# Kernel optimization log

Hardware: AMD Instinct MI355X
Metric: run time of the kernel (lower is better)

## Reference

```python
import jax, jax.numpy as jnp
import numpy as np

B, H, S, DK, DV = 4, 16, 2048, 64, 64
D_K = 64  # config.d_k used for scaling

def setup_inputs() -> dict:
    key = jax.random.key(0)
    kq, kk, kv, km = jax.random.split(key, 4)
    Q = jax.random.normal(kq, (B, H, S, DK), dtype=jnp.float32)
    K = jax.random.normal(kk, (B, H, S, DK), dtype=jnp.float32)
    V = jax.random.normal(kv, (B, H, S, DV), dtype=jnp.float32)
    attn_mask = jax.random.randint(km, (B, 1, S, S), 0, 2).astype(jnp.bool_)
    return {"Q": Q, "K": K, "V": V, "attn_mask": attn_mask}

def reference(Q, K, V, attn_mask):
    # scores: [B, H, S, S]
    scale = 1.0 / jnp.sqrt(jnp.asarray(D_K, dtype=Q.dtype))
    scores = jnp.einsum("bhqd,bhkd->bhqk", Q, K) * scale
    scores = jnp.where(attn_mask, jnp.asarray(-1e9, dtype=scores.dtype), scores)
    attn = jax.nn.softmax(scores, axis=-1)
    context = jnp.einsum("bhqk,bhkv->bhqv", attn, V)
    return context
```

## Files before the change

### kernel.cpp

```cpp
#include <hip/hip_runtime.h>
#include <hip/hip_bf16.h>
#include <math.h>

typedef __attribute__((ext_vector_type(4)))  float f32x4;
typedef __attribute__((ext_vector_type(16))) float f32x16;
typedef __attribute__((ext_vector_type(8)))  short short8_t;
typedef __attribute__((ext_vector_type(4)))  short short4_t;

constexpr int Bn = 4, Hn = 16, Sn = 2048, Dn = 64;
constexpr int MW  = Sn / 64;
constexpr int NKT = Sn / 64;

__device__ __forceinline__ unsigned short f2bf(float f) {
    union { float f; unsigned u; } x; x.f = f;
    unsigned r = x.u + 0x7fffu + ((x.u >> 16) & 1u);
    return (unsigned short)(r >> 16);
}
__device__ __forceinline__ int sw8(int row) { return (row ^ (row >> 3)) & 7; }
__device__ __forceinline__ float exp2fast(float x) {
#if __has_builtin(__builtin_amdgcn_exp2f)
    return __builtin_amdgcn_exp2f(x);
#else
    float r; asm("v_exp_f32 %0, %1" : "=v"(r) : "v"(x)); return r;
#endif
}
__device__ __forceinline__ float max3f(float a, float b, float c) {
    return fmaxf(fmaxf(a, b), c);
}
__device__ __forceinline__ f32x16 zero16() {
    f32x16 z;
#pragma unroll
    for (int i = 0; i < 16; ++i) z[i] = 0.f;
    return z;
}
__device__ __forceinline__ unsigned cvtpk(float lo, float hi_) {
    __hip_bfloat162 h2 = __float22bfloat162_rn(make_float2(lo, hi_));
    union { __hip_bfloat162 h; unsigned u; } u; u.h = h2;
    return u.u;
}
__device__ __forceinline__ void pswap(unsigned &x, unsigned &y) {
    asm("v_permlane32_swap_b32 %0, %1" : "+v"(x), "+v"(y));
}

__global__ __launch_bounds__(256) void pack_mask(const void* __restrict__ Mp,
                                                 unsigned long long* __restrict__ PM) {
    unsigned accv = 0;
    {
        const unsigned* mw = (const unsigned*)Mp;
#pragma unroll
        for (int i = 0; i < 8; ++i) accv |= (mw[i] & 0xFFFFFF00u);
    }
    const bool i32 = (accv == 0u);
    const int lane = threadIdx.x & 63;
    const int wv = (int)((blockIdx.x * 256 + threadIdx.x) >> 6);
    const int w0 = wv * (Bn * Sn * MW / 4096);
    const int* mi32 = (const int*)Mp;
    const unsigned char* mu8 = (const unsigned char*)Mp;
    for (int j = 0; j < 64; j += 4) {
        int m0, m1, m2, m3;
        if (i32) {
            m0 = mi32[(size_t)(w0 + j) * 64 + lane];
            m1 = mi32[(size_t)(w0 + j + 1) * 64 + lane];
            m2 = mi32[(size_t)(w0 + j + 2) * 64 + lane];
            m3 = mi32[(size_t)(w0 + j + 3) * 64 + lane];
        } else {
            m0 = mu8[(size_t)(w0 + j) * 64 + lane];
            m1 = mu8[(size_t)(w0 + j + 1) * 64 + lane];
            m2 = mu8[(size_t)(w0 + j + 2) * 64 + lane];
            m3 = mu8[(size_t)(w0 + j + 3) * 64 + lane];
        }
        unsigned long long b0 = __ballot(m0 != 0);
        unsigned long long b1 = __ballot(m1 != 0);
        unsigned long long b2 = __ballot(m2 != 0);
        unsigned long long b3 = __ballot(m3 != 0);
        if (lane == 0) {
            PM[w0 + j] = b0; PM[w0 + j + 1] = b1;
            PM[w0 + j + 2] = b2; PM[w0 + j + 3] = b3;
        }
    }
}

__global__ __launch_bounds__(256) void convKV(const float* __restrict__ K,
                                              const float* __restrict__ V,
                                              const void* __restrict__ Mp,
                                              unsigned short* __restrict__ Kb,
                                              unsigned short* __restrict__ Vt,
                                              unsigned long long* __restrict__ PM) {
    __shared__ unsigned short tile[64 * 72];
    const int bh = blockIdx.x, kt = blockIdx.y, t = threadIdx.x;

    {
        const float* ksrc = K + ((size_t)bh * Sn + kt * 64) * 64;
        unsigned short* kdst = Kb + ((size_t)bh * Sn + kt * 64) * 64;
#pragma unroll
        for (int j = 0; j < 2; ++j) {
            const int idx = j * 256 + t;
            f32x4 a = *(const f32x4*)(ksrc + idx * 8);
            f32x4 b = *(const f32x4*)(ksrc + idx * 8 + 4);
            short8_t h;
            h[0]=(short)f2bf(a[0]); h[1]=(short)f2bf(a[1]); h[2]=(short)f2bf(a[2]); h[3]=(short)f2bf(a[3]);
            h[4]=(short)f2bf(b[0]); h[5]=(short)f2bf(b[1]); h[6]=(short)f2bf(b[2]); h[7]=(short)f2bf(b[3]);
            *(short8_t*)(kdst + idx * 8) = h;
        }
    }

    {
        unsigned accv = 0;
        const unsigned* mw = (const unsigned*)Mp;
#pragma unroll
        for (int i = 0; i < 8; ++i) accv |= (mw[i] & 0xFFFFFF00u);
        const bool i32 = (accv == 0u);
        const int wv = t >> 6, lane = t & 63;
        const int base = (bh * NKT + kt) * 128 + wv * 32;
        const int* mi32 = (const int*)Mp;
        const unsigned char* mu8 = (const unsigned char*)Mp;
#pragma unroll 4
        for (int j = 0; j < 32; ++j) {
            int m = i32 ? mi32[(size_t)(base + j) * 64 + lane]
                        : (int)mu8[(size_t)(base + j) * 64 + lane];
            unsigned long long bal = __ballot(m != 0);
            if (lane == 0) PM[base + j] = bal;
        }
    }

    {
        const int k = t >> 2, vq = (t & 3) * 16;
        const float* src = V + ((size_t)bh * Sn + kt * 64 + k) * 64 + vq;
#pragma unroll
        for (int j = 0; j < 4; ++j) {
            f32x4 f = *(const f32x4*)(src + j * 4);
            short4_t h;
            h[0]=(short)f2bf(f[0]); h[1]=(short)f2bf(f[1]); h[2]=(short)f2bf(f[2]); h[3]=(short)f2bf(f[3]);
            *(short4_t*)&tile[k * 72 + vq + j * 4] = h;
        }
        __syncthreads();
#pragma unroll
        for (int j = 0; j < 2; ++j) {
            const int v = (t >> 3) + 32 * j;
            const int oct = t & 7;
            short8_t h;
#pragma unroll
            for (int i2 = 0; i2 < 8; ++i2) h[i2] = (short)tile[(oct * 8 + i2) * 72 + v];
            *(short8_t*)(Vt + ((size_t)bh * 64 + v) * Sn + kt * 64 + oct * 8) = h;
        }
    }
}

__global__ __launch_bounds__(256, 4) void sdpa_v3(
    const float* __restrict__ Qp, const unsigned short* __restrict__ Kb,
    const unsigned short* __restrict__ Vt, const unsigned long long* __restrict__ PM,
    float* __restrict__ Op)
{
    __shared__ __align__(16) char smem[32768];
    unsigned short* smK = (unsigned short*)smem;
    unsigned short* smV = (unsigned short*)(smem + 16384);
    unsigned short* smQ = (unsigned short*)smem;

    const int t = threadIdx.x;
    const int w = t >> 6;
    const int l = t & 63;
    const int ql = l & 31;
    const int hi = l >> 5;

    const int gid = blockIdx.x;
    const int lin = (gid & 7) * 128 + (gid >> 3);
    const int bh = lin >> 4;
    const int qb = lin & 15;
    const int b = bh >> 4;
    const int q0 = qb * 128;

    const unsigned short* KbB = Kb + (size_t)bh * Sn * 64;
    const unsigned short* VtB = Vt + (size_t)bh * 64 * Sn;

    {
        const float qscale = 0.125f * 1.44269504088896340736f;
        const float* Qbase = Qp + ((size_t)bh * Sn + q0) * Dn;
#pragma unroll
        for (int j = 0; j < 8; ++j) {
            const int flat = j * 256 + t;
            const int row = flat >> 4, c4 = (flat & 15) * 4;
            f32x4 f = *(const f32x4*)(Qbase + (size_t)flat * 4);
            short4_t h;
            h[0]=(short)f2bf(f[0]*qscale); h[1]=(short)f2bf(f[1]*qscale);
            h[2]=(short)f2bf(f[2]*qscale); h[3]=(short)f2bf(f[3]*qscale);
            *(short4_t*)&smQ[row * 72 + c4] = h;
        }
    }
    __syncthreads();
    short8_t qf[4];
    {
        const int rowl = w * 32 + ql;
#pragma unroll
        for (int tt = 0; tt < 4; ++tt)
            qf[tt] = *(const short8_t*)&smQ[rowl * 72 + tt * 16 + hi * 8];
    }
    __syncthreads();

    auto stage = [&](int kt, int buf) {
        const int row = t >> 3, oct = t & 7;
        const int row2 = row + 32;
        {
            const unsigned short* g = KbB + ((size_t)(kt * 64 + row)) * 64 + (oct ^ sw8(row)) * 8;
            __builtin_amdgcn_global_load_lds((const __attribute__((address_space(1))) unsigned int*)g,
                (__attribute__((address_space(3))) unsigned int*)(smK + buf * 4096 + t * 8), 16, 0, 0);
            const unsigned short* g2 = KbB + ((size_t)(kt * 64 + row2)) * 64 + (oct ^ sw8(row2)) * 8;
            __builtin_amdgcn_global_load_lds((const __attribute__((address_space(1))) unsigned int*)g2,
                (__attribute__((address_space(3))) unsigned int*)(smK + buf * 4096 + 2048 + t * 8), 16, 0, 0);
        }
        {
            const unsigned short* g = VtB + (size_t)row * Sn + kt * 64 + (oct ^ sw8(row)) * 8;
            __builtin_amdgcn_global_load_lds((const __attribute__((address_space(1))) unsigned int*)g,
                (__attribute__((address_space(3))) unsigned int*)(smV + buf * 4096 + t * 8), 16, 0, 0);
            const unsigned short* g2 = VtB + (size_t)row2 * Sn + kt * 64 + (oct ^ sw8(row2)) * 8;
            __builtin_amdgcn_global_load_lds((const __attribute__((address_space(1))) unsigned int*)g2,
                (__attribute__((address_space(3))) unsigned int*)(smV + buf * 4096 + 2048 + t * 8), 16, 0, 0);
        }
    };
    auto ldf = [&](const unsigned short* base, int row, int olog) -> short8_t {
        return *(const short8_t*)(base + row * 64 + (olog ^ sw8(row)) * 8);
    };

    f32x16 o0 = zero16(), o1 = zero16();
    float m_run = -INFINITY, l_run = 0.f;
    const int qrow = q0 + w * 32 + ql;
    const unsigned long long* pmrow = PM + ((size_t)b * Sn + qrow) * MW;

    stage(0, 0);
    __syncthreads();

    for (int kt = 0; kt < NKT; ++kt) {
        const int cur = kt & 1;
        if (kt + 1 < NKT) stage(kt + 1, cur ^ 1);
        const unsigned long long bits = pmrow[kt];
        const unsigned short* bK = smK + cur * 4096;
        const unsigned short* bV = smV + cur * 4096;

#pragma unroll
        for (int h = 0; h < 2; ++h) {
            f32x16 s = zero16();
            __builtin_amdgcn_s_setprio(1);
#pragma unroll
            for (int tt = 0; tt < 4; ++tt) {
                short8_t a0 = ldf(bK, 32 * h + ql, 2 * tt + hi);
                s = __builtin_amdgcn_mfma_f32_32x32x16_bf16(a0, qf[tt], s, 0, 0, 0);
            }
            __builtin_amdgcn_s_setprio(0);

            const unsigned w32 = (unsigned)(bits >> (32 * h)) >> (hi * 4);
#pragma unroll
            for (int r = 0; r < 16; ++r) {
                const int bp = 8 * (r >> 2) + (r & 3);
                s[r] = ((w32 >> bp) & 1u) ? -1e9f : s[r];
            }

            float mx = fmaxf(s[0], s[1]);
#pragma unroll
            for (int r = 2; r < 16; r += 2) mx = max3f(mx, s[r], s[r + 1]);
            mx = fmaxf(mx, __shfl_xor(mx, 32));

            if (!__all(mx - m_run <= 8.0f)) {
                const float mn = fmaxf(m_run, mx);
                const float corr = exp2fast(m_run - mn);
                m_run = mn;
                l_run *= corr;
#pragma unroll
                for (int r = 0; r < 16; ++r) {
                    const int qloc = (r & 3) + 8 * (r >> 2) + 4 * hi;
                    const float cr = __shfl(corr, qloc);
                    o0[r] *= cr; o1[r] *= cr;
                }
            }
#pragma unroll
            for (int r = 0; r < 16; ++r) s[r] = exp2fast(s[r] - m_run);

            {
                float p0 = 0.f, p1 = 0.f, p2 = 0.f, p3 = 0.f;
#pragma unroll
                for (int r = 0; r < 16; r += 4) {
                    p0 += s[r]; p1 += s[r + 1]; p2 += s[r + 2]; p3 += s[r + 3];
                }
                float rs = (p0 + p1) + (p2 + p3);
                rs += __shfl_xor(rs, 32);
                l_run += rs;
            }

            __builtin_amdgcn_s_setprio(1);
#pragma unroll
            for (int ksl = 0; ksl < 2; ++ksl) {
                const int off = ksl * 8;
                unsigned x0 = cvtpk(s[off],     s[off + 1]);
                unsigned x1 = cvtpk(s[off + 2], s[off + 3]);
                unsigned y0 = cvtpk(s[off + 4], s[off + 5]);
                unsigned y1 = cvtpk(s[off + 6], s[off + 7]);
                pswap(x0, y0);
                pswap(x1, y1);
                union { unsigned u[4]; short8_t v; } pa;
                pa.u[0] = x0; pa.u[1] = x1; pa.u[2] = y0; pa.u[3] = y1;
                const int ksg = 2 * h + ksl;
                short8_t vf0 = ldf(bV, ql,      2 * ksg + hi);
                short8_t vf1 = ldf(bV, 32 + ql, 2 * ksg + hi);
                o0 = __builtin_amdgcn_mfma_f32_32x32x16_bf16(pa.v, vf0, o0, 0, 0, 0);
                o1 = __builtin_amdgcn_mfma_f32_32x32x16_bf16(pa.v, vf1, o1, 0, 0, 0);
            }
            __builtin_amdgcn_s_setprio(0);
        }
        __syncthreads();
    }

    const float inv = 1.0f / l_run;
#pragma unroll
    for (int r = 0; r < 16; ++r) {
        const int qloc = (r & 3) + 8 * (r >> 2) + 4 * hi;
        const float iv = __shfl(inv, qloc);
        float* orow = Op + ((size_t)bh * Sn + q0 + w * 32 + qloc) * 64;
        orow[ql] = o0[r] * iv;
        orow[32 + ql] = o1[r] * iv;
    }
}

__global__ __launch_bounds__(512, 4) void sdpa_v2(
    const float* __restrict__ Qp, const float* __restrict__ Kp,
    const float* __restrict__ Vp, const void* __restrict__ Mp,
    const unsigned long long* __restrict__ PM, float* __restrict__ Op)
{
    __shared__ unsigned short lds_k[64 * 64];
    __shared__ unsigned short lds_vt[64 * 64];
    __shared__ unsigned short lds_p[8][16 * 64];

    const int t = threadIdx.x;
    const int wave = t >> 6;
    const int lane = t & 63;
    const int g = lane >> 4;
    const int c = lane & 15;

    const int gid = blockIdx.x;
    const int lin = (gid & 7) * 128 + (gid >> 3);
    const int bh = lin >> 4;
    const int qb = lin & 15;
    const int b = bh >> 4;
    const int q0 = qb * 128;

    bool m_i32 = true;
    if (!PM) {
        unsigned accv = 0;
        const unsigned* mw = (const unsigned*)Mp;
#pragma unroll
        for (int i = 0; i < 32; ++i) accv |= (mw[i] & 0xFFFFFF00u);
        m_i32 = (accv == 0u);
    }
    const int* mi32 = (const int*)Mp;
    const unsigned char* mu8 = (const unsigned char*)Mp;

    short8_t qf[2];
    {
        const float qscale = 0.125f * 1.44269504088896340736f;
        const float* qsrc = Qp + ((size_t)bh * Sn + q0 + wave * 16 + c) * Dn + g * 8;
#pragma unroll
        for (int h2 = 0; h2 < 2; ++h2) {
            f32x4 f0 = *(const f32x4*)(qsrc + h2 * 32);
            f32x4 f1 = *(const f32x4*)(qsrc + h2 * 32 + 4);
            short8_t v;
            v[0]=(short)f2bf(f0[0]*qscale); v[1]=(short)f2bf(f0[1]*qscale);
            v[2]=(short)f2bf(f0[2]*qscale); v[3]=(short)f2bf(f0[3]*qscale);
            v[4]=(short)f2bf(f1[0]*qscale); v[5]=(short)f2bf(f1[1]*qscale);
            v[6]=(short)f2bf(f1[2]*qscale); v[7]=(short)f2bf(f1[3]*qscale);
            qf[h2] = v;
        }
    }

    f32x4 o[4];
#pragma unroll
    for (int i = 0; i < 4; ++i) o[i] = (f32x4){0.f, 0.f, 0.f, 0.f};
    float m_run[4] = {-INFINITY, -INFINITY, -INFINITY, -INFINITY};
    float l_run[4] = {0.f, 0.f, 0.f, 0.f};

    const float* kbase = Kp + (size_t)bh * Sn * Dn;
    const float* vbase = Vp + (size_t)bh * Sn * Dn;
    const size_t mrow0 = (size_t)b * Sn + q0 + wave * 16 + g * 4;

    for (int kt = 0; kt < NKT; ++kt) {
        const int k0 = kt * 64;
        {
            const int key = t >> 3;
            const int d0 = (t & 7) * 8;
            const float* src = kbase + (size_t)(k0 + key) * Dn + d0;
            f32x4 f0 = *(const f32x4*)src;
            f32x4 f1 = *(const f32x4*)(src + 4);
            short8_t hv;
            hv[0]=(short)f2bf(f0[0]); hv[1]=(short)f2bf(f0[1]);
            hv[2]=(short)f2bf(f0[2]); hv[3]=(short)f2bf(f0[3]);
            hv[4]=(short)f2bf(f1[0]); hv[5]=(short)f2bf(f1[1]);
            hv[6]=(short)f2bf(f1[2]); hv[7]=(short)f2bf(f1[3]);
            *(short8_t*)&lds_k[key * 64 + (d0 ^ (sw8(key) << 3))] = hv;
        }
        {
            const int vv = t & 63;
            const int kq = (t >> 6) * 8;
            short8_t hv;
#pragma unroll
            for (int j = 0; j < 8; ++j)
                hv[j] = (short)f2bf(vbase[(size_t)(k0 + kq + j) * Dn + vv]);
            *(short8_t*)&lds_vt[vv * 64 + (kq ^ (sw8(vv) << 3))] = hv;
        }
        __syncthreads();

        f32x4 s[4];
#pragma unroll
        for (int e = 0; e < 4; ++e) s[e] = (f32x4){0.f, 0.f, 0.f, 0.f};
        __builtin_amdgcn_s_setprio(1);
#pragma unroll
        for (int e = 0; e < 4; ++e) {
            const int ke = e * 16 + c;
            const int swk = sw8(ke) << 3;
            short8_t kf0 = *(const short8_t*)&lds_k[ke * 64 + ((g * 8) ^ swk)];
            short8_t kf1 = *(const short8_t*)&lds_k[ke * 64 + ((32 + g * 8) ^ swk)];
            s[e] = __builtin_amdgcn_mfma_f32_16x16x32_bf16(qf[0], kf0, s[e], 0, 0, 0);
            s[e] = __builtin_amdgcn_mfma_f32_16x16x32_bf16(qf[1], kf1, s[e], 0, 0, 0);
        }
        __builtin_amdgcn_s_setprio(0);

        unsigned long long bits[4];
        if (PM) {
#pragma unroll
            for (int r = 0; r < 4; ++r) bits[r] = PM[(mrow0 + r) * MW + kt];
        } else {
#pragma unroll
            for (int r = 0; r < 4; ++r) {
                const size_t mi = (mrow0 + r) * Sn + k0 + c;
                unsigned long long bbv = 0;
#pragma unroll
                for (int e = 0; e < 4; ++e) {
                    int mm = m_i32 ? mi32[mi + 16 * e] : (int)mu8[mi + 16 * e];
                    bbv |= (unsigned long long)(mm != 0) << (c + 16 * e);
                }
                bits[r] = bbv;
            }
        }

        float p[4][4], mx[4];
#pragma unroll
        for (int r = 0; r < 4; ++r) {
            const unsigned lo = (unsigned)bits[r];
            const unsigned hh = (unsigned)(bits[r] >> 32);
            const unsigned t0 = lo >> c;
            const unsigned t1 = hh >> c;
            float v0 = (t0 & 1u)       ? -1e9f : s[0][r];
            float v1 = (t0 & 0x10000u) ? -1e9f : s[1][r];
            float v2 = (t1 & 1u)       ? -1e9f : s[2][r];
            float v3 = (t1 & 0x10000u) ? -1e9f : s[3][r];
            p[0][r] = v0; p[1][r] = v1; p[2][r] = v2; p[3][r] = v3;
            mx[r] = fmaxf(fmaxf(v0, v1), fmaxf(v2, v3));
        }
#pragma unroll
        for (int sh = 1; sh < 16; sh <<= 1) {
#pragma unroll
            for (int r = 0; r < 4; ++r) mx[r] = fmaxf(mx[r], __shfl_xor(mx[r], sh));
        }
        float need = mx[0] - m_run[0];
        need = fmaxf(need, mx[1] - m_run[1]);
        need = fmaxf(need, mx[2] - m_run[2]);
        need = fmaxf(need, mx[3] - m_run[3]);
        if (!__all(need <= 8.0f)) {
#pragma unroll
            for (int r = 0; r < 4; ++r) {
                const float mn = fmaxf(m_run[r], mx[r]);
                const float corr = exp2fast(m_run[r] - mn);
                m_run[r] = mn;
                l_run[r] *= corr;
#pragma unroll
                for (int cg = 0; cg < 4; ++cg) o[cg][r] *= corr;
            }
        }
        float rsv[4];
#pragma unroll
        for (int r = 0; r < 4; ++r) {
            p[0][r] = exp2fast(p[0][r] - m_run[r]);
            p[1][r] = exp2fast(p[1][r] - m_run[r]);
            p[2][r] = exp2fast(p[2][r] - m_run[r]);
            p[3][r] = exp2fast(p[3][r] - m_run[r]);
            rsv[r] = (p[0][r] + p[1][r]) + (p[2][r] + p[3][r]);
        }
#pragma unroll
        for (int sh = 1; sh < 16; sh <<= 1) {
#pragma unroll
            for (int r = 0; r < 4; ++r) rsv[r] += __shfl_xor(rsv[r], sh);
        }
#pragma unroll
        for (int r = 0; r < 4; ++r) l_run[r] += rsv[r];

        unsigned short* pw = lds_p[wave];
#pragma unroll
        for (int r = 0; r < 4; ++r) {
            const int row = g * 4 + r;
            const int swp = sw8(row) << 3;
            pw[row * 64 + ((c)      ^ swp)] = f2bf(p[0][r]);
            pw[row * 64 + ((c + 16) ^ swp)] = f2bf(p[1][r]);
            pw[row * 64 + ((c + 32) ^ swp)] = f2bf(p[2][r]);
            pw[row * 64 + ((c + 48) ^ swp)] = f2bf(p[3][r]);
        }
        const int swc = sw8(c) << 3;
        const short8_t pf0 = *(const short8_t*)&pw[c * 64 + ((g * 8) ^ swc)];
        const short8_t pf1 = *(const short8_t*)&pw[c * 64 + ((32 + g * 8) ^ swc)];
        __builtin_amdgcn_s_setprio(1);
#pragma unroll
        for (int cg = 0; cg < 4; ++cg) {
            const int vv = cg * 16 + c;
            const int swv = sw8(vv) << 3;
            const short8_t vf0 = *(const short8_t*)&lds_vt[vv * 64 + ((g * 8) ^ swv)];
            const short8_t vf1 = *(const short8_t*)&lds_vt[vv * 64 + ((32 + g * 8) ^ swv)];
            o[cg] = __builtin_amdgcn_mfma_f32_16x16x32_bf16(pf0, vf0, o[cg], 0, 0, 0);
            o[cg] = __builtin_amdgcn_mfma_f32_16x16x32_bf16(pf1, vf1, o[cg], 0, 0, 0);
        }
        __builtin_amdgcn_s_setprio(0);
        __syncthreads();
    }

#pragma unroll
    for (int r = 0; r < 4; ++r) {
        const float inv = 1.0f / l_run[r];
        float* orow = Op + ((size_t)bh * Sn + q0 + wave * 16 + g * 4 + r) * Dn + c;
#pragma unroll
        for (int cg = 0; cg < 4; ++cg) orow[cg * 16] = o[cg][r] * inv;
    }
}

extern "C" void kernel_launch(void* const* d_in, const int* in_sizes, int n_in,
                              void* d_out, int out_size, void* d_ws, size_t ws_size,
                              hipStream_t stream) {
    (void)in_sizes; (void)n_in; (void)out_size;
    const float* Q = (const float*)d_in[0];
    const float* K = (const float*)d_in[1];
    const float* V = (const float*)d_in[2];
    const void*  M = d_in[3];
    float* O = (float*)d_out;

    const size_t pmB = (size_t)Bn * Sn * MW * 8;
    const size_t kvB = (size_t)Bn * Hn * Sn * Dn * 2;

    if (ws_size >= pmB + 2 * kvB) {
        unsigned long long* PM = (unsigned long long*)d_ws;
        unsigned short* Kb = (unsigned short*)((char*)d_ws + pmB);
        unsigned short* Vt = (unsigned short*)((char*)d_ws + pmB + kvB);
        convKV<<<dim3(Bn * Hn, NKT), 256, 0, stream>>>(K, V, M, Kb, Vt, PM);
        sdpa_v3<<<dim3(1024), dim3(256), 0, stream>>>(Q, Kb, Vt, PM, O);
    } else {
        unsigned long long* PM = nullptr;
        if (ws_size >= pmB) {
            PM = (unsigned long long*)d_ws;
            pack_mask<<<1024, 256, 0, stream>>>(M, PM);
        }
        sdpa_v2<<<dim3(1024), dim3(512), 0, stream>>>(Q, K, V, M, PM, O);
    }
}
```

Baseline: 143.1 us.

## Double query tile per block to 256 rows with 8 waves sharing K/V stages

The flash-attention block grows from 4 to 8 waves, so each block covers 256 query rows and the grid halves to 512 blocks. Each K/V tile staged into LDS is now reused by twice as many waves, and each thread issues one async global-to-LDS load per tensor instead of two. Q is loaded straight from global memory into registers and converted to bf16 per lane, removing the LDS round trip and two barriers, and the first K/V stage is issued before the Q load to overlap them. The trade-offs are larger blocks with 8-wave barriers, fewer blocks for load balancing, and possible register pressure under launch_bounds(512,4).

New measurement: 140.1 us. 1.02x faster.

```diff
diff --git a/kernel.cpp b/kernel.cpp
--- a/kernel.cpp
+++ b/kernel.cpp
@@ -146,7 +146,7 @@
     }
 }
 
-__global__ __launch_bounds__(256, 4) void sdpa_v3(
+__global__ __launch_bounds__(512, 4) void sdpa_v3(
     const float* __restrict__ Qp, const unsigned short* __restrict__ Kb,
     const unsigned short* __restrict__ Vt, const unsigned long long* __restrict__ PM,
     float* __restrict__ Op)
@@ -154,7 +154,6 @@
     __shared__ __align__(16) char smem[32768];
     unsigned short* smK = (unsigned short*)smem;
     unsigned short* smV = (unsigned short*)(smem + 16384);
-    unsigned short* smQ = (unsigned short*)smem;
 
     const int t = threadIdx.x;
     const int w = t >> 6;
@@ -163,69 +162,56 @@
     const int hi = l >> 5;
 
     const int gid = blockIdx.x;
-    const int lin = (gid & 7) * 128 + (gid >> 3);
-    const int bh = lin >> 4;
-    const int qb = lin & 15;
+    const int lin = (gid & 7) * 64 + (gid >> 3);
+    const int bh = lin >> 3;
+    const int qb = lin & 7;
     const int b = bh >> 4;
-    const int q0 = qb * 128;
+    const int q0 = qb * 256;
 
     const unsigned short* KbB = Kb + (size_t)bh * Sn * 64;
     const unsigned short* VtB = Vt + (size_t)bh * 64 * Sn;
 
-    {
-        const float qscale = 0.125f * 1.44269504088896340736f;
-        const float* Qbase = Qp + ((size_t)bh * Sn + q0) * Dn;
-#pragma unroll
-        for (int j = 0; j < 8; ++j) {
-            const int flat = j * 256 + t;
-            const int row = flat >> 4, c4 = (flat & 15) * 4;
-            f32x4 f = *(const f32x4*)(Qbase + (size_t)flat * 4);
-            short4_t h;
-            h[0]=(short)f2bf(f[0]*qscale); h[1]=(short)f2bf(f[1]*qscale);
-            h[2]=(short)f2bf(f[2]*qscale); h[3]=(short)f2bf(f[3]*qscale);
-            *(short4_t*)&smQ[row * 72 + c4] = h;
-        }
-    }
-    __syncthreads();
-    short8_t qf[4];
-    {
-        const int rowl = w * 32 + ql;
-#pragma unroll
-        for (int tt = 0; tt < 4; ++tt)
-            qf[tt] = *(const short8_t*)&smQ[rowl * 72 + tt * 16 + hi * 8];
-    }
-    __syncthreads();
-
     auto stage = [&](int kt, int buf) {
         const int row = t >> 3, oct = t & 7;
-        const int row2 = row + 32;
         {
             const unsigned short* g = KbB + ((size_t)(kt * 64 + row)) * 64 + (oct ^ sw8(row)) * 8;
             __builtin_amdgcn_global_load_lds((const __attribute__((address_space(1))) unsigned int*)g,
                 (__attribute__((address_space(3))) unsigned int*)(smK + buf * 4096 + t * 8), 16, 0, 0);
-            const unsigned short* g2 = KbB + ((size_t)(kt * 64 + row2)) * 64 + (oct ^ sw8(row2)) * 8;
-            __builtin_amdgcn_global_load_lds((const __attribute__((address_space(1))) unsigned int*)g2,
-                (__attribute__((address_space(3))) unsigned int*)(smK + buf * 4096 + 2048 + t * 8), 16, 0, 0);
         }
         {
             const unsigned short* g = VtB + (size_t)row * Sn + kt * 64 + (oct ^ sw8(row)) * 8;
             __builtin_amdgcn_global_load_lds((const __attribute__((address_space(1))) unsigned int*)g,
                 (__attribute__((address_space(3))) unsigned int*)(smV + buf * 4096 + t * 8), 16, 0, 0);
-            const unsigned short* g2 = VtB + (size_t)row2 * Sn + kt * 64 + (oct ^ sw8(row2)) * 8;
-            __builtin_amdgcn_global_load_lds((const __attribute__((address_space(1))) unsigned int*)g2,
-                (__attribute__((address_space(3))) unsigned int*)(smV + buf * 4096 + 2048 + t * 8), 16, 0, 0);
         }
     };
     auto ldf = [&](const unsigned short* base, int row, int olog) -> short8_t {
         return *(const short8_t*)(base + row * 64 + (olog ^ sw8(row)) * 8);
     };
 
+    stage(0, 0);
+
+    short8_t qf[4];
+    {
+        const float qscale = 0.125f * 1.44269504088896340736f;
+        const float* qsrc = Qp + ((size_t)bh * Sn + q0 + w * 32 + ql) * Dn + hi * 8;
+#pragma unroll
+        for (int tt = 0; tt < 4; ++tt) {
+            f32x4 f0 = *(const f32x4*)(qsrc + tt * 16);
+            f32x4 f1 = *(const f32x4*)(qsrc + tt * 16 + 4);
+            short8_t v;
+            v[0]=(short)f2bf(f0[0]*qscale); v[1]=(short)f2bf(f0[1]*qscale);
+            v[2]=(short)f2bf(f0[2]*qscale); v[3]=(short)f2bf(f0[3]*qscale);
+            v[4]=(short)f2bf(f1[0]*qscale); v[5]=(short)f2bf(f1[1]*qscale);
+            v[6]=(short)f2bf(f1[2]*qscale); v[7]=(short)f2bf(f1[3]*qscale);
+            qf[tt] = v;
+        }
+    }
+
     f32x16 o0 = zero16(), o1 = zero16();
     float m_run = -INFINITY, l_run = 0.f;
     const int qrow = q0 + w * 32 + ql;
     const unsigned long long* pmrow = PM + ((size_t)b * Sn + qrow) * MW;
 
-    stage(0, 0);
     __syncthreads();
 
     for (int kt = 0; kt < NKT; ++kt) {
@@ -542,7 +528,7 @@
         unsigned short* Kb = (unsigned short*)((char*)d_ws + pmB);
         unsigned short* Vt = (unsigned short*)((char*)d_ws + pmB + kvB);
         convKV<<<dim3(Bn * Hn, NKT), 256, 0, stream>>>(K, V, M, Kb, Vt, PM);
-        sdpa_v3<<<dim3(1024), dim3(256), 0, stream>>>(Q, Kb, Vt, PM, O);
+        sdpa_v3<<<dim3(512), dim3(512), 0, stream>>>(Q, Kb, Vt, PM, O);
     } else {
         unsigned long long* PM = nullptr;
         if (ws_size >= pmB) {
```
